# Performance work log

Hardware: AMD Instinct MI355X
Metric: run time of the kernel (lower is better)

The kernel has to match this reference:

```python
import jax, jax.numpy as jnp
import numpy as np

N, D, N_CLASSES = 8192, 512, 128
POS_MARGIN = 1.0  # default path: sample_method=None, Dynamic_margin=None


def setup_inputs() -> dict:
    key = jax.random.key(0)
    k1, k2 = jax.random.split(key)
    x = jax.random.normal(k1, (N, D), dtype=jnp.float32)
    # metric-learning embeddings are L2-normalized so sim in [-1, 1]
    x = x / jnp.linalg.norm(x, axis=1, keepdims=True)
    targets = jax.random.randint(k2, (N,), 0, N_CLASSES, dtype=jnp.int64)
    return {"inputs": x, "targets": targets, "nonorm": 0}


def reference(inputs, targets, nonorm):
    n = inputs.shape[0]
    sim = jnp.matmul(inputs, inputs.T)                      # [n, n]
    same = targets[:, None] == targets[None, :]             # [n, n]
    pos_mask = same & (sim < POS_MARGIN)                    # drops self-sim == 1
    neg_mask = ~same

    # per-row masked log-sum-exp (sort in original is irrelevant to the sums)
    pos_sum = jnp.sum(jnp.where(pos_mask, jnp.exp(1.0 - sim), 0.0), axis=1)
    neg_sum = jnp.sum(jnp.where(neg_mask, jnp.exp(sim), 0.0), axis=1)
    pos_loss = jnp.log(pos_sum)
    neg_loss = jnp.log(neg_sum)

    has_neg = jnp.any(neg_mask, axis=1)                     # rows w/o negs are skipped
    loss = jnp.sum(jnp.where(has_neg, pos_loss + neg_loss, 0.0)) / n
    prec = jnp.mean(1.0 - has_neg.astype(jnp.float32))      # fraction of skipped rows

    # torch code reports means of the LAST row's pos/neg pairs
    last_pos = pos_mask[-1]
    last_neg = neg_mask[-1]
    mean_pos_sim = jnp.sum(jnp.where(last_pos, sim[-1], 0.0)) / jnp.sum(last_pos)
    mean_neg_sim = jnp.sum(jnp.where(last_neg, sim[-1], 0.0)) / jnp.sum(last_neg)
    return loss, prec, mean_pos_sim, mean_neg_sim
```

## Files before the change

kernel.cpp:

```cpp
#include <hip/hip_runtime.h>
#include <math.h>

#define N_ 8192
#define D_ 512
#define NC_ 128
#define T_ 64
#define BK_ 32
#define KSTEPS 16

typedef __attribute__((ext_vector_type(8))) short bf16x8;
typedef __attribute__((ext_vector_type(4))) float f32x4;
typedef __attribute__((ext_vector_type(4))) unsigned short us4;

static __device__ __forceinline__ unsigned short f2bf(float f) {
    union { float f; unsigned u; } c; c.f = f;
    unsigned u = c.u;
    u += 0x7fffu + ((u >> 16) & 1u);
    return (unsigned short)(u >> 16);
}

__global__ __launch_bounds__(256) void k_pre(const float* __restrict__ x,
                                             unsigned short* __restrict__ xb,
                                             const int* __restrict__ tg,
                                             double* __restrict__ sim_last,
                                             int* __restrict__ hist32,
                                             double* __restrict__ gd,
                                             int* __restrict__ gi) {
    const int bid = blockIdx.x;
    const int tid = threadIdx.x;
    if (bid == 0 && tid == 0) {
        atomicExch((unsigned long long*)&gd[0], 0ull);
        atomicExch((unsigned long long*)&gd[1], 0ull);
        atomicExch((unsigned long long*)&gd[2], 0ull);
        atomicExch(&gi[0], 0); atomicExch(&gi[1], 0);
        atomicExch(&gi[2], 0); atomicExch(&gi[3], 0);
    }
    if (bid < 4096) {
        int i = bid * 256 + tid;
        float4 v = reinterpret_cast<const float4*>(x)[i];
        us4 o = { f2bf(v.x), f2bf(v.y), f2bf(v.z), f2bf(v.w) };
        reinterpret_cast<us4*>(xb)[i] = o;
    } else if (bid < 6144) {
        int j    = (bid - 4096) * 4 + (tid >> 6);
        int lane = tid & 63;
        const float* xl = x + (size_t)(N_ - 1) * D_;
        const float* xj = x + (size_t)j * D_;
        double acc = 0.0;
#pragma unroll
        for (int it = 0; it < 8; ++it) {
            int k = it * 64 + lane;
            acc += (double)xl[k] * (double)xj[k];
        }
#pragma unroll
        for (int m = 32; m >= 1; m >>= 1) acc += __shfl_xor(acc, m, 64);
        if (lane == 0) sim_last[j] = acc;
    } else {
        __shared__ int lh[NC_];
        int b = bid - 6144;
        if (tid < NC_) lh[tid] = 0;
        __syncthreads();
        atomicAdd(&lh[tg[b * 256 + tid]], 1);
        __syncthreads();
        if (tid < NC_) hist32[b * NC_ + tid] = lh[tid];
    }
}

__global__ __launch_bounds__(256, 4) void k_main(const unsigned short* __restrict__ xb,
                                                 const int* __restrict__ tg,
                                                 float* __restrict__ bufP,
                                                 float* __restrict__ bufN) {
    __shared__ alignas(16) unsigned short As[2][128 * BK_];
    __shared__ alignas(16) unsigned short Bs[2][128 * BK_];

    const int tid  = threadIdx.x;
    const int w    = tid >> 6;
    const int lane = tid & 63;
    const int q    = lane >> 4;
    const int l15  = lane & 15;
    const int wrow = w >> 1;
    const int wcol = w & 1;

    const int bswz = (blockIdx.x & 7) * 260 + (blockIdx.x >> 3);

    int rem = bswz;
    int it = 0;
    while (rem >= (T_ - it)) { rem -= (T_ - it); it++; }
    const int jt = it + rem;
    const int row0 = it * 128;
    const int col0 = jt * 128;

    auto stage_tile = [&](int p, int kt) {
        const int k0 = kt * BK_;
#pragma unroll
        for (int itr = 0; itr < 2; ++itr) {
            int slot = itr * 4 + w;
            int gs = slot * 64 + lane;
            int r  = gs >> 2;
            int sl = gs & 3;
            int g  = sl ^ ((r >> 1) & 3);
            const unsigned short* ga = xb + (size_t)(row0 + r) * D_ + k0 + g * 8;
            const unsigned short* gb = xb + (size_t)(col0 + r) * D_ + k0 + g * 8;
            __builtin_amdgcn_global_load_lds(
                (const __attribute__((address_space(1))) void*)ga,
                (__attribute__((address_space(3))) void*)(&As[p][0] + slot * 512),
                16, 0, 0);
            __builtin_amdgcn_global_load_lds(
                (const __attribute__((address_space(1))) void*)gb,
                (__attribute__((address_space(3))) void*)(&Bs[p][0] + slot * 512),
                16, 0, 0);
        }
    };

    f32x4 acc[4][4];
#pragma unroll
    for (int mi = 0; mi < 4; ++mi)
#pragma unroll
        for (int ni = 0; ni < 4; ++ni)
            acc[mi][ni] = (f32x4){0.f, 0.f, 0.f, 0.f};

    auto compute_tile = [&](int p) {
        bf16x8 aF[4], bF[4];
#pragma unroll
        for (int mi = 0; mi < 4; ++mi) {
            int rA = wrow * 64 + mi * 16 + l15;
            int sl = q ^ ((rA >> 1) & 3);
            aF[mi] = *reinterpret_cast<const bf16x8*>(&As[p][0] + rA * BK_ + sl * 8);
        }
#pragma unroll
        for (int ni = 0; ni < 4; ++ni) {
            int rB = wcol * 64 + ni * 16 + l15;
            int sl = q ^ ((rB >> 1) & 3);
            bF[ni] = *reinterpret_cast<const bf16x8*>(&Bs[p][0] + rB * BK_ + sl * 8);
        }
        asm volatile("s_waitcnt lgkmcnt(0)" ::: "memory");
        __builtin_amdgcn_sched_barrier(0);
        __builtin_amdgcn_s_setprio(1);
#pragma unroll
        for (int mi = 0; mi < 4; ++mi)
#pragma unroll
            for (int ni = 0; ni < 4; ++ni)
                acc[mi][ni] = __builtin_amdgcn_mfma_f32_16x16x32_bf16(
                    aF[mi], bF[ni], acc[mi][ni], 0, 0, 0);
        __builtin_amdgcn_s_setprio(0);
    };

#define TILE(P, KS, DOSTAGE, VMN)                                         \
    do {                                                                  \
        asm volatile("s_waitcnt vmcnt(" #VMN ")" ::: "memory");           \
        __builtin_amdgcn_s_barrier();                                     \
        __builtin_amdgcn_sched_barrier(0);                                \
        compute_tile(P);                                                  \
        __builtin_amdgcn_s_barrier();                                     \
        __builtin_amdgcn_sched_barrier(0);                                \
        if (DOSTAGE) stage_tile(P, (KS) + 2);                             \
    } while (0)

    stage_tile(0, 0);
    stage_tile(1, 1);

    TILE(0, 0, 1, 4);
    TILE(1, 1, 1, 4);
    TILE(0, 2, 1, 4);
    TILE(1, 3, 1, 4);
    TILE(0, 4, 1, 4);
    TILE(1, 5, 1, 4);
    TILE(0, 6, 1, 4);
    TILE(1, 7, 1, 4);
    TILE(0, 8, 1, 4);
    TILE(1, 9, 1, 4);
    TILE(0, 10, 1, 4);
    TILE(1, 11, 1, 4);
    TILE(0, 12, 1, 4);
    TILE(1, 13, 1, 4);
    TILE(0, 14, 0, 4);
    TILE(1, 15, 0, 0);
#undef TILE

    int tC[4];
#pragma unroll
    for (int ni = 0; ni < 4; ++ni)
        tC[ni] = tg[col0 + wcol * 64 + ni * 16 + l15];

    float ps[4][4], ns[4][4];
    float cps[4], cns[4];
    int tR[4][4];
#pragma unroll
    for (int mi = 0; mi < 4; ++mi)
#pragma unroll
        for (int r = 0; r < 4; ++r) {
            ps[mi][r] = 0.f; ns[mi][r] = 0.f;
            tR[mi][r] = tg[row0 + wrow * 64 + mi * 16 + q * 4 + r];
        }
#pragma unroll
    for (int ni = 0; ni < 4; ++ni) { cps[ni] = 0.f; cns[ni] = 0.f; }

#pragma unroll
    for (int mi = 0; mi < 4; ++mi)
#pragma unroll
        for (int ni = 0; ni < 4; ++ni)
#pragma unroll
            for (int r = 0; r < 4; ++r) {
                float s = acc[mi][ni][r];
                bool same = (tR[mi][r] == tC[ni]);
                float e = __expf(same ? 1.0f - s : s);
                float pe = (same && (s < 1.0f)) ? e : 0.0f;
                float ne = same ? 0.0f : e;
                ps[mi][r] += pe; ns[mi][r] += ne;
                cps[ni]   += pe; cns[ni]   += ne;
            }

    float* scr = (float*)As;
#pragma unroll
    for (int mi = 0; mi < 4; ++mi)
#pragma unroll
        for (int r = 0; r < 4; ++r) {
            float p = ps[mi][r];
            float n = ns[mi][r];
#pragma unroll
            for (int m = 1; m < 16; m <<= 1) {
                p += __shfl_xor(p, m, 64);
                n += __shfl_xor(n, m, 64);
            }
            if (l15 == 0) {
                int rloc = wrow * 64 + mi * 16 + q * 4 + r;
                scr[wcol * 128 + rloc]       = p;
                scr[256 + wcol * 128 + rloc] = n;
            }
        }

#pragma unroll
    for (int ni = 0; ni < 4; ++ni) {
        float p = cps[ni];
        float n = cns[ni];
        p += __shfl_xor(p, 16, 64); p += __shfl_xor(p, 32, 64);
        n += __shfl_xor(n, 16, 64); n += __shfl_xor(n, 32, 64);
        if (q == 0) {
            int cloc = wcol * 64 + ni * 16 + l15;
            scr[512 + wrow * 128 + cloc] = p;
            scr[768 + wrow * 128 + cloc] = n;
        }
    }
    __syncthreads();

    if (tid < 128) {
        int r = tid;
        size_t off = ((size_t)it * T_ + jt) * 128 + r;
        bufP[off] = scr[r]       + scr[128 + r];
        bufN[off] = scr[256 + r] + scr[384 + r];
    } else if (jt != it) {
        int c = tid - 128;
        size_t off = ((size_t)jt * T_ + it) * 128 + c;
        bufP[off] = scr[512 + c] + scr[640 + c];
        bufN[off] = scr[768 + c] + scr[896 + c];
    }
}

__global__ __launch_bounds__(256) void k_post(const float* __restrict__ bufP,
                                              const float* __restrict__ bufN,
                                              const int* __restrict__ tg,
                                              const int* __restrict__ hist32,
                                              const double* __restrict__ sim_last,
                                              double* __restrict__ gd,
                                              int* __restrict__ gi,
                                              float* __restrict__ out) {
    __shared__ int lh[NC_];
    __shared__ float sv[256];
    __shared__ double Rd[256], Pd[256], Nd[256];
    __shared__ int Ri[256], Pc[256], Nc[256];
    const int t   = blockIdx.x;
    const int tid = threadIdx.x;

    if (tid < NC_) {
        int a = 0;
#pragma unroll
        for (int b = 0; b < 32; ++b) a += hist32[b * NC_ + tid];
        lh[tid] = a;
    }

    const int half = tid >> 7;
    const int r    = tid & 127;
    const float* buf  = half ? bufN : bufP;
    const float* base = buf + (size_t)t * T_ * 128 + r;
    float s = 0.f;
#pragma unroll
    for (int o = 0; o < T_; ++o) s += base[o * 128];
    sv[tid] = s;
    __syncthreads();

    double rd = 0.0, pd = 0.0, nd = 0.0;
    int ri = 0, pc = 0, nc = 0;
    if (tid < 128) {
        int row = t * 128 + tid;
        bool ok = lh[tg[row]] < N_;
        rd = ok ? (double)(logf(sv[tid]) + logf(sv[128 + tid])) : 0.0;
        ri = ok ? 0 : 1;
        double sl = sim_last[row];
        int tlast = tg[N_ - 1];
        if (tg[row] == tlast) { if (sl < 1.0) { pd = sl; pc = 1; } }
        else                  { nd = sl; nc = 1; }
    }

    Rd[tid] = rd; Ri[tid] = ri;
    Pd[tid] = pd; Pc[tid] = pc;
    Nd[tid] = nd; Nc[tid] = nc;
    __syncthreads();
    for (int st = 128; st >= 1; st >>= 1) {
        if (tid < st) {
            Rd[tid] += Rd[tid + st]; Pd[tid] += Pd[tid + st]; Nd[tid] += Nd[tid + st];
            Ri[tid] += Ri[tid + st]; Pc[tid] += Pc[tid + st]; Nc[tid] += Nc[tid + st];
        }
        __syncthreads();
    }

    if (tid == 0) {
        atomicAdd(&gd[0], Rd[0]);
        atomicAdd(&gd[1], Pd[0]);
        atomicAdd(&gd[2], Nd[0]);
        atomicAdd(&gi[0], Ri[0]);
        atomicAdd(&gi[1], Pc[0]);
        atomicAdd(&gi[2], Nc[0]);
        __threadfence();
        int old = atomicAdd(&gi[3], 1);
        if (old == 63) {
            double A = atomicAdd(&gd[0], 0.0);
            double B = atomicAdd(&gd[1], 0.0);
            double C = atomicAdd(&gd[2], 0.0);
            int U = atomicAdd(&gi[0], 0);
            int V = atomicAdd(&gi[1], 0);
            int Y = atomicAdd(&gi[2], 0);
            out[0] = (float)(A / (double)N_);
            out[1] = (float)U / (float)N_;
            out[2] = (float)(B / (double)V);
            out[3] = (float)(C / (double)Y);
        }
    }
}

extern "C" void kernel_launch(void* const* d_in, const int* in_sizes, int n_in,
                              void* d_out, int out_size, void* d_ws, size_t ws_size,
                              hipStream_t stream) {
    const float* x  = (const float*)d_in[0];
    const int*   tg = (const int*)d_in[1];
    char* ws = (char*)d_ws;

    unsigned short* xb = (unsigned short*)ws;
    const size_t XB = (size_t)N_ * D_ * 2;
    float*  bufP = (float*)(ws + XB);
    float*  bufN = (float*)(ws + XB + 2097152);
    double* sim_last = (double*)(ws + XB + 4194304);
    int*    hist32   = (int*)(ws + XB + 4194304 + 65536);
    double* gd   = (double*)(ws + XB + 4194304 + 65536 + 16384);
    int*    gi   = (int*)(ws + XB + 4194304 + 65536 + 16384 + 64);

    const int nblk_tri = T_ * (T_ + 1) / 2;

    hipLaunchKernelGGL(k_pre, dim3(4096 + 2048 + 32), dim3(256), 0, stream,
                       x, xb, tg, sim_last, hist32, gd, gi);
    hipLaunchKernelGGL(k_main, dim3(nblk_tri), dim3(256), 0, stream, xb, tg, bufP, bufN);
    hipLaunchKernelGGL(k_post, dim3(64), dim3(256), 0, stream,
                       bufP, bufN, tg, hist32, sim_last, gd, gi, (float*)d_out);
}
```

Before: 147.1 us.

## Persistent blocks with LDS-resident A row panel over chunks of column tiles

Replaces the one-block-per-triangular-tile launch with 256 persistent blocks that take chunks of up to four column tiles from an atomic work counter. Each chunk loads the full 128x512 A row panel into LDS once and reuses it across the chunk, streaming only B tiles double-buffered, with the next tile's first B loads prefetched. The aim is to cut A-panel global/L2 traffic and launch tail imbalance. In exchange, occupancy drops to one block per CU because of the large LDS footprint, and the A panel load at each chunk start is not overlapped with compute.

Result: slower. 216.8 us (+47.4%).

```diff
diff --git a/kernel.cpp b/kernel.cpp
--- a/kernel.cpp
+++ b/kernel.cpp
@@ -6,7 +6,8 @@
 #define NC_ 128
 #define T_ 64
 #define BK_ 32
-#define KSTEPS 16
+#define KT_ 16
+#define NCHUNK 544
 
 typedef __attribute__((ext_vector_type(8))) short bf16x8;
 typedef __attribute__((ext_vector_type(4))) float f32x4;
@@ -34,6 +35,7 @@
         atomicExch((unsigned long long*)&gd[2], 0ull);
         atomicExch(&gi[0], 0); atomicExch(&gi[1], 0);
         atomicExch(&gi[2], 0); atomicExch(&gi[3], 0);
+        atomicExch(&gi[4], 256);
     }
     if (bid < 4096) {
         int i = bid * 256 + tid;
@@ -65,12 +67,15 @@
     }
 }
 
-__global__ __launch_bounds__(256, 4) void k_main(const unsigned short* __restrict__ xb,
+__global__ __launch_bounds__(256, 1) void k_main(const unsigned short* __restrict__ xb,
                                                  const int* __restrict__ tg,
                                                  float* __restrict__ bufP,
-                                                 float* __restrict__ bufN) {
-    __shared__ alignas(16) unsigned short As[2][128 * BK_];
+                                                 float* __restrict__ bufN,
+                                                 int* __restrict__ gi) {
+    __shared__ alignas(16) unsigned short A_lds[KT_][128 * BK_];
     __shared__ alignas(16) unsigned short Bs[2][128 * BK_];
+    __shared__ float scr[1024];
+    __shared__ int sh_next;
 
     const int tid  = threadIdx.x;
     const int w    = tid >> 6;
@@ -80,17 +85,8 @@
     const int wrow = w >> 1;
     const int wcol = w & 1;
 
-    const int bswz = (blockIdx.x & 7) * 260 + (blockIdx.x >> 3);
-
-    int rem = bswz;
-    int it = 0;
-    while (rem >= (T_ - it)) { rem -= (T_ - it); it++; }
-    const int jt = it + rem;
-    const int row0 = it * 128;
-    const int col0 = jt * 128;
-
-    auto stage_tile = [&](int p, int kt) {
-        const int k0 = kt * BK_;
+    auto stage_arr = [&](unsigned short* dst, const unsigned short* src_base,
+                         int r0, int k0) {
 #pragma unroll
         for (int itr = 0; itr < 2; ++itr) {
             int slot = itr * 4 + w;
@@ -98,39 +94,31 @@
             int r  = gs >> 2;
             int sl = gs & 3;
             int g  = sl ^ ((r >> 1) & 3);
-            const unsigned short* ga = xb + (size_t)(row0 + r) * D_ + k0 + g * 8;
-            const unsigned short* gb = xb + (size_t)(col0 + r) * D_ + k0 + g * 8;
+            const unsigned short* ga = src_base + (size_t)(r0 + r) * D_ + k0 + g * 8;
             __builtin_amdgcn_global_load_lds(
                 (const __attribute__((address_space(1))) void*)ga,
-                (__attribute__((address_space(3))) void*)(&As[p][0] + slot * 512),
+                (__attribute__((address_space(3))) void*)(dst + slot * 512),
                 16, 0, 0);
-            __builtin_amdgcn_global_load_lds(
-                (const __attribute__((address_space(1))) void*)gb,
-                (__attribute__((address_space(3))) void*)(&Bs[p][0] + slot * 512),
-                16, 0, 0);
         }
     };
 
     f32x4 acc[4][4];
-#pragma unroll
-    for (int mi = 0; mi < 4; ++mi)
-#pragma unroll
-        for (int ni = 0; ni < 4; ++ni)
-            acc[mi][ni] = (f32x4){0.f, 0.f, 0.f, 0.f};
-
-    auto compute_tile = [&](int p) {
+
+    auto compute_tile = [&](int kt) {
+        const unsigned short* A = &A_lds[kt][0];
+        const unsigned short* B = &Bs[kt & 1][0];
         bf16x8 aF[4], bF[4];
 #pragma unroll
         for (int mi = 0; mi < 4; ++mi) {
             int rA = wrow * 64 + mi * 16 + l15;
             int sl = q ^ ((rA >> 1) & 3);
-            aF[mi] = *reinterpret_cast<const bf16x8*>(&As[p][0] + rA * BK_ + sl * 8);
+            aF[mi] = *reinterpret_cast<const bf16x8*>(A + rA * BK_ + sl * 8);
         }
 #pragma unroll
         for (int ni = 0; ni < 4; ++ni) {
             int rB = wcol * 64 + ni * 16 + l15;
             int sl = q ^ ((rB >> 1) & 3);
-            bF[ni] = *reinterpret_cast<const bf16x8*>(&Bs[p][0] + rB * BK_ + sl * 8);
+            bF[ni] = *reinterpret_cast<const bf16x8*>(B + rB * BK_ + sl * 8);
         }
         asm volatile("s_waitcnt lgkmcnt(0)" ::: "memory");
         __builtin_amdgcn_sched_barrier(0);
@@ -144,114 +132,129 @@
         __builtin_amdgcn_s_setprio(0);
     };
 
-#define TILE(P, KS, DOSTAGE, VMN)                                         \
-    do {                                                                  \
-        asm volatile("s_waitcnt vmcnt(" #VMN ")" ::: "memory");           \
-        __builtin_amdgcn_s_barrier();                                     \
-        __builtin_amdgcn_sched_barrier(0);                                \
-        compute_tile(P);                                                  \
-        __builtin_amdgcn_s_barrier();                                     \
-        __builtin_amdgcn_sched_barrier(0);                                \
-        if (DOSTAGE) stage_tile(P, (KS) + 2);                             \
-    } while (0)
-
-    stage_tile(0, 0);
-    stage_tile(1, 1);
-
-    TILE(0, 0, 1, 4);
-    TILE(1, 1, 1, 4);
-    TILE(0, 2, 1, 4);
-    TILE(1, 3, 1, 4);
-    TILE(0, 4, 1, 4);
-    TILE(1, 5, 1, 4);
-    TILE(0, 6, 1, 4);
-    TILE(1, 7, 1, 4);
-    TILE(0, 8, 1, 4);
-    TILE(1, 9, 1, 4);
-    TILE(0, 10, 1, 4);
-    TILE(1, 11, 1, 4);
-    TILE(0, 12, 1, 4);
-    TILE(1, 13, 1, 4);
-    TILE(0, 14, 0, 4);
-    TILE(1, 15, 0, 0);
-#undef TILE
-
-    int tC[4];
-#pragma unroll
-    for (int ni = 0; ni < 4; ++ni)
-        tC[ni] = tg[col0 + wcol * 64 + ni * 16 + l15];
-
-    float ps[4][4], ns[4][4];
-    float cps[4], cns[4];
-    int tR[4][4];
-#pragma unroll
-    for (int mi = 0; mi < 4; ++mi)
-#pragma unroll
-        for (int r = 0; r < 4; ++r) {
-            ps[mi][r] = 0.f; ns[mi][r] = 0.f;
-            tR[mi][r] = tg[row0 + wrow * 64 + mi * 16 + q * 4 + r];
-        }
-#pragma unroll
-    for (int ni = 0; ni < 4; ++ni) { cps[ni] = 0.f; cns[ni] = 0.f; }
-
-#pragma unroll
-    for (int mi = 0; mi < 4; ++mi)
-#pragma unroll
-        for (int ni = 0; ni < 4; ++ni)
-#pragma unroll
-            for (int r = 0; r < 4; ++r) {
-                float s = acc[mi][ni][r];
-                bool same = (tR[mi][r] == tC[ni]);
-                float e = __expf(same ? 1.0f - s : s);
-                float pe = (same && (s < 1.0f)) ? e : 0.0f;
-                float ne = same ? 0.0f : e;
-                ps[mi][r] += pe; ns[mi][r] += ne;
-                cps[ni]   += pe; cns[ni]   += ne;
+    int id = blockIdx.x;
+    while (id < NCHUNK) {
+        int rem = id, it = 0;
+        while (rem >= ((T_ - it + 3) >> 2)) { rem -= (T_ - it + 3) >> 2; it++; }
+        const int jt0 = it + rem * 4;
+        const int len = min(4, T_ - it - rem * 4);
+        const int row0 = it * 128;
+
+#pragma unroll 1
+        for (int kt = 0; kt < KT_; ++kt)
+            stage_arr(&A_lds[kt][0], xb, row0, kt * BK_);
+        stage_arr(&Bs[0][0], xb, jt0 * 128, 0);
+        stage_arr(&Bs[1][0], xb, jt0 * 128, BK_);
+
+#pragma unroll 1
+        for (int j = 0; j < len; ++j) {
+            const int jt   = jt0 + j;
+            const int col0 = jt * 128;
+            const bool has_next = (j < len - 1);
+
+#pragma unroll
+            for (int mi = 0; mi < 4; ++mi)
+#pragma unroll
+                for (int ni = 0; ni < 4; ++ni)
+                    acc[mi][ni] = (f32x4){0.f, 0.f, 0.f, 0.f};
+
+#pragma unroll 1
+            for (int kt = 0; kt < KT_; ++kt) {
+                asm volatile("s_waitcnt vmcnt(2)" ::: "memory");
+                __builtin_amdgcn_s_barrier();
+                __builtin_amdgcn_sched_barrier(0);
+                compute_tile(kt);
+                __builtin_amdgcn_s_barrier();
+                __builtin_amdgcn_sched_barrier(0);
+                if (kt < KT_ - 2) {
+                    stage_arr(&Bs[kt & 1][0], xb, col0, (kt + 2) * BK_);
+                } else if (has_next) {
+                    stage_arr(&Bs[kt & 1][0], xb, col0 + 128, (kt & 1) * BK_);
+                }
             }
 
-    float* scr = (float*)As;
-#pragma unroll
-    for (int mi = 0; mi < 4; ++mi)
-#pragma unroll
-        for (int r = 0; r < 4; ++r) {
-            float p = ps[mi][r];
-            float n = ns[mi][r];
-#pragma unroll
-            for (int m = 1; m < 16; m <<= 1) {
-                p += __shfl_xor(p, m, 64);
-                n += __shfl_xor(n, m, 64);
+            int tC[4];
+#pragma unroll
+            for (int ni = 0; ni < 4; ++ni)
+                tC[ni] = tg[col0 + wcol * 64 + ni * 16 + l15];
+
+            float ps[4][4], ns[4][4];
+            float cps[4], cns[4];
+            int tR[4][4];
+#pragma unroll
+            for (int mi = 0; mi < 4; ++mi)
+#pragma unroll
+                for (int r = 0; r < 4; ++r) {
+                    ps[mi][r] = 0.f; ns[mi][r] = 0.f;
+                    tR[mi][r] = tg[row0 + wrow * 64 + mi * 16 + q * 4 + r];
+                }
+#pragma unroll
+            for (int ni = 0; ni < 4; ++ni) { cps[ni] = 0.f; cns[ni] = 0.f; }
+
+#pragma unroll
+            for (int mi = 0; mi < 4; ++mi)
+#pragma unroll
+                for (int ni = 0; ni < 4; ++ni)
+#pragma unroll
+                    for (int r = 0; r < 4; ++r) {
+                        float s = acc[mi][ni][r];
+                        bool same = (tR[mi][r] == tC[ni]);
+                        float e = __expf(same ? 1.0f - s : s);
+                        float pe = (same && (s < 1.0f)) ? e : 0.0f;
+                        float ne = same ? 0.0f : e;
+                        ps[mi][r] += pe; ns[mi][r] += ne;
+                        cps[ni]   += pe; cns[ni]   += ne;
+                    }
+
+#pragma unroll
+            for (int mi = 0; mi < 4; ++mi)
+#pragma unroll
+                for (int r = 0; r < 4; ++r) {
+                    float p = ps[mi][r];
+                    float n = ns[mi][r];
+#pragma unroll
+                    for (int m = 1; m < 16; m <<= 1) {
+                        p += __shfl_xor(p, m, 64);
+                        n += __shfl_xor(n, m, 64);
+                    }
+                    if (l15 == 0) {
+                        int rloc = wrow * 64 + mi * 16 + q * 4 + r;
+                        scr[wcol * 128 + rloc]       = p;
+                        scr[256 + wcol * 128 + rloc] = n;
+                    }
+                }
+
+#pragma unroll
+            for (int ni = 0; ni < 4; ++ni) {
+                float p = cps[ni];
+                float n = cns[ni];
+                p += __shfl_xor(p, 16, 64); p += __shfl_xor(p, 32, 64);
+                n += __shfl_xor(n, 16, 64); n += __shfl_xor(n, 32, 64);
+                if (q == 0) {
+                    int cloc = wcol * 64 + ni * 16 + l15;
+                    scr[512 + wrow * 128 + cloc] = p;
+                    scr[768 + wrow * 128 + cloc] = n;
+                }
             }
-            if (l15 == 0) {
-                int rloc = wrow * 64 + mi * 16 + q * 4 + r;
-                scr[wcol * 128 + rloc]       = p;
-                scr[256 + wcol * 128 + rloc] = n;
+            __syncthreads();
+
+            if (tid < 128) {
+                int r = tid;
+                size_t off = ((size_t)it * T_ + jt) * 128 + r;
+                bufP[off] = scr[r]       + scr[128 + r];
+                bufN[off] = scr[256 + r] + scr[384 + r];
+            } else if (jt != it) {
+                int c = tid - 128;
+                size_t off = ((size_t)jt * T_ + it) * 128 + c;
+                bufP[off] = scr[512 + c] + scr[640 + c];
+                bufN[off] = scr[768 + c] + scr[896 + c];
             }
-        }
-
-#pragma unroll
-    for (int ni = 0; ni < 4; ++ni) {
-        float p = cps[ni];
-        float n = cns[ni];
-        p += __shfl_xor(p, 16, 64); p += __shfl_xor(p, 32, 64);
-        n += __shfl_xor(n, 16, 64); n += __shfl_xor(n, 32, 64);
-        if (q == 0) {
-            int cloc = wcol * 64 + ni * 16 + l15;
-            scr[512 + wrow * 128 + cloc] = p;
-            scr[768 + wrow * 128 + cloc] = n;
-        }
-    }
-    __syncthreads();
-
-    if (tid < 128) {
-        int r = tid;
-        size_t off = ((size_t)it * T_ + jt) * 128 + r;
-        bufP[off] = scr[r]       + scr[128 + r];
-        bufN[off] = scr[256 + r] + scr[384 + r];
-    } else if (jt != it) {
-        int c = tid - 128;
-        size_t off = ((size_t)jt * T_ + it) * 128 + c;
-        bufP[off] = scr[512 + c] + scr[640 + c];
-        bufN[off] = scr[768 + c] + scr[896 + c];
+            __syncthreads();
+        }
+
+        if (tid == 0) sh_next = atomicAdd(&gi[4], 1);
+        __syncthreads();
+        id = sh_next;
     }
 }
 
@@ -352,11 +355,10 @@
     double* gd   = (double*)(ws + XB + 4194304 + 65536 + 16384);
     int*    gi   = (int*)(ws + XB + 4194304 + 65536 + 16384 + 64);
 
-    const int nblk_tri = T_ * (T_ + 1) / 2;
-
     hipLaunchKernelGGL(k_pre, dim3(4096 + 2048 + 32), dim3(256), 0, stream,
                        x, xb, tg, sim_last, hist32, gd, gi);
-    hipLaunchKernelGGL(k_main, dim3(nblk_tri), dim3(256), 0, stream, xb, tg, bufP, bufN);
+    hipLaunchKernelGGL(k_main, dim3(256), dim3(256), 0, stream,
+                       xb, tg, bufP, bufN, gi);
     hipLaunchKernelGGL(k_post, dim3(64), dim3(256), 0, stream,
                        bufP, bufN, tg, hist32, sim_last, gd, gi, (float*)d_out);
 }
```

## Fuse post-reduction into main kernel via last-blocks-done atomic counter

Applied to the files above, without the earlier changes.

Removes the separate k_post launch by having each k_main block increment a global counter after writing its partials. The last 64 blocks to arrive spin until all blocks finish, then each performs one row-tile's final reduction and loss accumulation, reusing the shared memory. This saves a kernel launch and its gap, at the cost of spin-waiting blocks and a dependence on those 64 blocks staying co-resident while waiting.

New measurement: 360.0 us. 2.45x slower.

```diff
diff --git a/kernel.cpp b/kernel.cpp
--- a/kernel.cpp
+++ b/kernel.cpp
@@ -7,6 +7,7 @@
 #define T_ 64
 #define BK_ 32
 #define KSTEPS 16
+#define NBLK 2080
 
 typedef __attribute__((ext_vector_type(8))) short bf16x8;
 typedef __attribute__((ext_vector_type(4))) float f32x4;
@@ -34,6 +35,7 @@
         atomicExch((unsigned long long*)&gd[2], 0ull);
         atomicExch(&gi[0], 0); atomicExch(&gi[1], 0);
         atomicExch(&gi[2], 0); atomicExch(&gi[3], 0);
+        atomicExch(&gi[5], 0);
     }
     if (bid < 4096) {
         int i = bid * 256 + tid;
@@ -68,9 +70,15 @@
 __global__ __launch_bounds__(256, 4) void k_main(const unsigned short* __restrict__ xb,
                                                  const int* __restrict__ tg,
                                                  float* __restrict__ bufP,
-                                                 float* __restrict__ bufN) {
+                                                 float* __restrict__ bufN,
+                                                 const int* __restrict__ hist32,
+                                                 const double* __restrict__ sim_last,
+                                                 double* __restrict__ gd,
+                                                 int* __restrict__ gi,
+                                                 float* __restrict__ out) {
     __shared__ alignas(16) unsigned short As[2][128 * BK_];
     __shared__ alignas(16) unsigned short Bs[2][128 * BK_];
+    __shared__ int sh_fin;
 
     const int tid  = threadIdx.x;
     const int w    = tid >> 6;
@@ -253,85 +261,94 @@
         bufP[off] = scr[512 + c] + scr[640 + c];
         bufN[off] = scr[768 + c] + scr[896 + c];
     }
-}
-
-__global__ __launch_bounds__(256) void k_post(const float* __restrict__ bufP,
-                                              const float* __restrict__ bufN,
-                                              const int* __restrict__ tg,
-                                              const int* __restrict__ hist32,
-                                              const double* __restrict__ sim_last,
-                                              double* __restrict__ gd,
-                                              int* __restrict__ gi,
-                                              float* __restrict__ out) {
-    __shared__ int lh[NC_];
-    __shared__ float sv[256];
-    __shared__ double Rd[256], Pd[256], Nd[256];
-    __shared__ int Ri[256], Pc[256], Nc[256];
-    const int t   = blockIdx.x;
-    const int tid = threadIdx.x;
-
-    if (tid < NC_) {
-        int a = 0;
-#pragma unroll
-        for (int b = 0; b < 32; ++b) a += hist32[b * NC_ + tid];
-        lh[tid] = a;
-    }
-
-    const int half = tid >> 7;
-    const int r    = tid & 127;
-    const float* buf  = half ? bufN : bufP;
-    const float* base = buf + (size_t)t * T_ * 128 + r;
-    float s = 0.f;
-#pragma unroll
-    for (int o = 0; o < T_; ++o) s += base[o * 128];
-    sv[tid] = s;
+
+    __threadfence();
     __syncthreads();
-
-    double rd = 0.0, pd = 0.0, nd = 0.0;
-    int ri = 0, pc = 0, nc = 0;
-    if (tid < 128) {
-        int row = t * 128 + tid;
-        bool ok = lh[tg[row]] < N_;
-        rd = ok ? (double)(logf(sv[tid]) + logf(sv[128 + tid])) : 0.0;
-        ri = ok ? 0 : 1;
-        double sl = sim_last[row];
-        int tlast = tg[N_ - 1];
-        if (tg[row] == tlast) { if (sl < 1.0) { pd = sl; pc = 1; } }
-        else                  { nd = sl; nc = 1; }
-    }
-
-    Rd[tid] = rd; Ri[tid] = ri;
-    Pd[tid] = pd; Pc[tid] = pc;
-    Nd[tid] = nd; Nc[tid] = nc;
+    if (tid == 0) sh_fin = atomicAdd(&gi[5], 1);
     __syncthreads();
-    for (int st = 128; st >= 1; st >>= 1) {
-        if (tid < st) {
-            Rd[tid] += Rd[tid + st]; Pd[tid] += Pd[tid + st]; Nd[tid] += Nd[tid + st];
-            Ri[tid] += Ri[tid + st]; Pc[tid] += Pc[tid + st]; Nc[tid] += Nc[tid + st];
-        }
+    const int fin = sh_fin - (NBLK - 64);
+    if (fin < 0) return;
+
+    if (tid == 0) {
+        while (atomicAdd(&gi[5], 0) < NBLK) __builtin_amdgcn_s_sleep(8);
+    }
+    __syncthreads();
+    __threadfence();
+
+    {
+        const int t = fin;
+        int*    lh = (int*)&As[0][0];
+        float*  sv = (float*)((char*)&As[0][0] + 512);
+        double* Rd = (double*)((char*)&As[0][0] + 1536);
+        double* Pd = Rd + 256;
+        double* Nd = Pd + 256;
+        int*    Ri = (int*)(Nd + 256);
+        int*    Pc = Ri + 256;
+        int*    Nc = Pc + 256;
+
+        if (tid < NC_) {
+            int a = 0;
+#pragma unroll
+            for (int b = 0; b < 32; ++b) a += hist32[b * NC_ + tid];
+            lh[tid] = a;
+        }
+
+        const int half = tid >> 7;
+        const int r    = tid & 127;
+        const float* buf  = half ? bufN : bufP;
+        const float* base = buf + (size_t)t * T_ * 128 + r;
+        float s = 0.f;
+#pragma unroll
+        for (int o = 0; o < T_; ++o) s += base[o * 128];
+        sv[tid] = s;
         __syncthreads();
-    }
-
-    if (tid == 0) {
-        atomicAdd(&gd[0], Rd[0]);
-        atomicAdd(&gd[1], Pd[0]);
-        atomicAdd(&gd[2], Nd[0]);
-        atomicAdd(&gi[0], Ri[0]);
-        atomicAdd(&gi[1], Pc[0]);
-        atomicAdd(&gi[2], Nc[0]);
-        __threadfence();
-        int old = atomicAdd(&gi[3], 1);
-        if (old == 63) {
-            double A = atomicAdd(&gd[0], 0.0);
-            double B = atomicAdd(&gd[1], 0.0);
-            double C = atomicAdd(&gd[2], 0.0);
-            int U = atomicAdd(&gi[0], 0);
-            int V = atomicAdd(&gi[1], 0);
-            int Y = atomicAdd(&gi[2], 0);
-            out[0] = (float)(A / (double)N_);
-            out[1] = (float)U / (float)N_;
-            out[2] = (float)(B / (double)V);
-            out[3] = (float)(C / (double)Y);
+
+        double rd = 0.0, pd = 0.0, nd = 0.0;
+        int ri = 0, pc = 0, nc = 0;
+        if (tid < 128) {
+            int row = t * 128 + tid;
+            bool ok = lh[tg[row]] < N_;
+            rd = ok ? (double)(logf(sv[tid]) + logf(sv[128 + tid])) : 0.0;
+            ri = ok ? 0 : 1;
+            double sl = sim_last[row];
+            int tlast = tg[N_ - 1];
+            if (tg[row] == tlast) { if (sl < 1.0) { pd = sl; pc = 1; } }
+            else                  { nd = sl; nc = 1; }
+        }
+
+        Rd[tid] = rd; Ri[tid] = ri;
+        Pd[tid] = pd; Pc[tid] = pc;
+        Nd[tid] = nd; Nc[tid] = nc;
+        __syncthreads();
+        for (int st = 128; st >= 1; st >>= 1) {
+            if (tid < st) {
+                Rd[tid] += Rd[tid + st]; Pd[tid] += Pd[tid + st]; Nd[tid] += Nd[tid + st];
+                Ri[tid] += Ri[tid + st]; Pc[tid] += Pc[tid + st]; Nc[tid] += Nc[tid + st];
+            }
+            __syncthreads();
+        }
+
+        if (tid == 0) {
+            atomicAdd(&gd[0], Rd[0]);
+            atomicAdd(&gd[1], Pd[0]);
+            atomicAdd(&gd[2], Nd[0]);
+            atomicAdd(&gi[0], Ri[0]);
+            atomicAdd(&gi[1], Pc[0]);
+            atomicAdd(&gi[2], Nc[0]);
+            __threadfence();
+            int old = atomicAdd(&gi[3], 1);
+            if (old == 63) {
+                double A = atomicAdd(&gd[0], 0.0);
+                double B = atomicAdd(&gd[1], 0.0);
+                double C = atomicAdd(&gd[2], 0.0);
+                int U = atomicAdd(&gi[0], 0);
+                int V = atomicAdd(&gi[1], 0);
+                int Y = atomicAdd(&gi[2], 0);
+                out[0] = (float)(A / (double)N_);
+                out[1] = (float)U / (float)N_;
+                out[2] = (float)(B / (double)V);
+                out[3] = (float)(C / (double)Y);
+            }
         }
     }
 }
@@ -352,11 +369,8 @@
     double* gd   = (double*)(ws + XB + 4194304 + 65536 + 16384);
     int*    gi   = (int*)(ws + XB + 4194304 + 65536 + 16384 + 64);
 
-    const int nblk_tri = T_ * (T_ + 1) / 2;
-
     hipLaunchKernelGGL(k_pre, dim3(4096 + 2048 + 32), dim3(256), 0, stream,
                        x, xb, tg, sim_last, hist32, gd, gi);
-    hipLaunchKernelGGL(k_main, dim3(nblk_tri), dim3(256), 0, stream, xb, tg, bufP, bufN);
-    hipLaunchKernelGGL(k_post, dim3(64), dim3(256), 0, stream,
-                       bufP, bufN, tg, hist32, sim_last, gd, gi, (float*)d_out);
+    hipLaunchKernelGGL(k_main, dim3(NBLK), dim3(256), 0, stream,
+                       xb, tg, bufP, bufN, hist32, sim_last, gd, gi, (float*)d_out);
 }
```
